# Optimization experiments

Measured on AMD Instinct MI355X. Metric: run time of the kernel, lower is better.

The kernel has to match this reference:

```python
import jax, jax.numpy as jnp
import numpy as np

N_NODES = 50000
HIDDEN = 256
N_EDGES = 300000


def setup_inputs() -> dict:
    key = jax.random.key(0)
    k1, k2, k3, k4 = jax.random.split(key, 4)
    node_embeddings = jax.random.normal(k1, (N_NODES, HIDDEN), dtype=jnp.float32)
    edge_weights_index = jax.random.randint(k2, (2, N_EDGES), 0, N_NODES, dtype=jnp.int64)
    # lin1: Linear(2H -> H), lin2: Linear(H -> 1); jax convention [in, out]
    W1 = jax.random.normal(k3, (2 * HIDDEN, HIDDEN), dtype=jnp.float32) * (1.0 / np.sqrt(2 * HIDDEN))
    b1 = jnp.zeros((HIDDEN,), dtype=jnp.float32)
    W2 = jax.random.normal(k4, (HIDDEN, 1), dtype=jnp.float32) * (1.0 / np.sqrt(HIDDEN))
    b2 = jnp.zeros((1,), dtype=jnp.float32)
    return {"node_embeddings": node_embeddings, "edge_weights_index": edge_weights_index,
            "W1": W1, "b1": b1, "W2": W2, "b2": b2}


def reference(node_embeddings, edge_weights_index, W1, b1, W2, b2):
    src = edge_weights_index[0, :]
    trg = edge_weights_index[1, :]
    # Split W1 into src/trg halves: concat([s, t]) @ W1 == s @ W1s + t @ W1t.
    # Avoids materializing the [E, 2H] concatenated edge tensor.
    W1s, W1t = W1[:HIDDEN], W1[HIDDEN:]
    h = node_embeddings[src] @ W1s + node_embeddings[trg] @ W1t + b1  # [E, H]
    h = jax.nn.relu(h)
    prediction = h @ W2 + b2  # [E, 1]
    return prediction.reshape(-1)
```

## Files before the change

kernel.cpp:

```cpp
#include <hip/hip_runtime.h>
#include <hip/hip_bf16.h>

#define N_NODES 50000
#define HID     256
#define N_EDGES 300000
#define NT      32
#define NTILES  ((N_NODES + NT - 1) / NT)

typedef __attribute__((ext_vector_type(8))) short bf16x8;
typedef __attribute__((ext_vector_type(4))) float f32x4;

__device__ __forceinline__ unsigned short f2bf(float f) {
  unsigned int u = __float_as_uint(f);
  u = (u + 0x7FFFu + ((u >> 16) & 1u)) >> 16;
  return (unsigned short)u;
}
__device__ __forceinline__ float bflo(unsigned int u) { return __uint_as_float(u << 16); }
__device__ __forceinline__ float bfhi(unsigned int u) { return __uint_as_float(u & 0xFFFF0000u); }

__device__ __forceinline__ bf16x8 cvt8(float4 u, float4 v) {
  bf16x8 r;
  r[0] = (short)f2bf(u.x); r[1] = (short)f2bf(u.y);
  r[2] = (short)f2bf(u.z); r[3] = (short)f2bf(u.w);
  r[4] = (short)f2bf(v.x); r[5] = (short)f2bf(v.y);
  r[6] = (short)f2bf(v.z); r[7] = (short)f2bf(v.w);
  return r;
}

struct StageRegs { float4 a, b, c, d; };

__device__ __forceinline__ void load_tile(const float* __restrict__ E, int tile,
                                          int srow, int sg, StageRegs& s) {
  int grow = tile * NT + srow;
  if (grow < N_NODES) {
    const float4* p = reinterpret_cast<const float4*>(E + (size_t)grow * HID + sg * 8);
    s.a = p[0]; s.b = p[1]; s.c = p[32]; s.d = p[33];
  } else {
    s.a = s.b = s.c = s.d = make_float4(0.f, 0.f, 0.f, 0.f);
  }
}

__global__ __launch_bounds__(128) void pack_w_kernel(
    const float* __restrict__ W1, unsigned short* __restrict__ Wtf) {
  int k = blockIdx.x;
  int t = threadIdx.x;
  int half = t >> 6;
  int jj = (t & 63) * 4;
  const float4 v = *reinterpret_cast<const float4*>(
      W1 + (size_t)(half ? (HID + k) : k) * HID + jj);
  float vv[4] = {v.x, v.y, v.z, v.w};
#pragma unroll
  for (int e = 0; e < 4; ++e) {
    int j = half * HID + jj + e;
    int f    = (j >> 4) * 8 + (k >> 5);
    int lane = (j & 15) | (((k >> 3) & 3) << 4);
    int elem = k & 7;
    Wtf[f * 512 + lane * 8 + elem] = f2bf(vv[e]);
  }
}

__global__ __launch_bounds__(512, 2) void gemm_kernel(
    const float* __restrict__ E, const unsigned short* __restrict__ Wtf,
    const float* __restrict__ b1, unsigned short* __restrict__ P) {
  __shared__ alignas(16) char lds0[16384];
  __shared__ alignas(16) char lds1[16384];
  const int tid  = threadIdx.x;
  const int lane = tid & 63;
  const int w    = tid >> 6;

  bf16x8 a[4][8];
#pragma unroll
  for (int m = 0; m < 4; ++m)
#pragma unroll
    for (int kk = 0; kk < 8; ++kk)
      a[m][kk] = *reinterpret_cast<const bf16x8*>(
          Wtf + (((size_t)(w * 4 + m) * 8 + kk) << 9) + lane * 8);

  float4 bv[4];
#pragma unroll
  for (int m = 0; m < 4; ++m) {
    int fm = w * 4 + m;
    bv[m] = (fm < 16) ? *reinterpret_cast<const float4*>(b1 + fm * 16 + ((lane >> 4) << 2))
                      : make_float4(0.f, 0.f, 0.f, 0.f);
  }

  const int srow = tid >> 4;
  const int sg   = tid & 15;
  const int woff0 = srow * 512 + ((sg * 16) ^ ((srow & 7) << 4));
  const int woff1 = srow * 512 + (((sg + 16) * 16) ^ ((srow & 7) << 4));
  const int G = gridDim.x;

  auto write_tile = [&](char* buf, const StageRegs& s) {
    *reinterpret_cast<bf16x8*>(&buf[woff0]) = cvt8(s.a, s.b);
    *reinterpret_cast<bf16x8*>(&buf[woff1]) = cvt8(s.c, s.d);
  };

  auto compute_store = [&](const char* buf, int tt) {
    f32x4 acc[4][2] = {};
#pragma unroll
    for (int n = 0; n < 2; ++n) {
      int r   = n * 16 + (lane & 15);
      int rb  = r * 512;
      int sw  = (r & 7) << 4;
      int kb0 = (lane >> 4) << 4;
      bf16x8 bfr[8];
#pragma unroll
      for (int kk = 0; kk < 8; ++kk)
        bfr[kk] = *reinterpret_cast<const bf16x8*>(&buf[rb + ((kk * 64 + kb0) ^ sw)]);
#pragma unroll
      for (int kk = 0; kk < 8; ++kk)
#pragma unroll
        for (int m = 0; m < 4; ++m)
          acc[m][n] = __builtin_amdgcn_mfma_f32_16x16x32_bf16(a[m][kk], bfr[kk], acc[m][n], 0, 0, 0);
    }
#pragma unroll
    for (int m = 0; m < 4; ++m) {
      int pcb = (w * 4 + m) * 16 + ((lane >> 4) << 2);
#pragma unroll
      for (int n = 0; n < 2; ++n) {
        int node = tt * NT + n * 16 + (lane & 15);
        if (node < N_NODES) {
          ushort4 o;
          o.x = f2bf(acc[m][n][0] + bv[m].x);
          o.y = f2bf(acc[m][n][1] + bv[m].y);
          o.z = f2bf(acc[m][n][2] + bv[m].z);
          o.w = f2bf(acc[m][n][3] + bv[m].w);
          *reinterpret_cast<ushort4*>(P + (size_t)node * 512 + pcb) = o;
        }
      }
    }
  };

  int t = blockIdx.x;
  StageRegs sX, sY;
  load_tile(E, t, srow, sg, sX);
  if (t + G < NTILES) load_tile(E, t + G, srow, sg, sY);
  write_tile(lds0, sX);
  if (t + 2 * G < NTILES) load_tile(E, t + 2 * G, srow, sg, sX);
  __syncthreads();

  while (true) {
    compute_store(lds0, t);
    if (t + G >= NTILES) break;
    write_tile(lds1, sY);
    if (t + 3 * G < NTILES) load_tile(E, t + 3 * G, srow, sg, sY);
    __syncthreads();
    t += G;
    compute_store(lds1, t);
    if (t + G >= NTILES) break;
    write_tile(lds0, sX);
    if (t + 3 * G < NTILES) load_tile(E, t + 3 * G, srow, sg, sX);
    __syncthreads();
    t += G;
  }
}

__global__ __launch_bounds__(256) void edge_kernel(
    const int* __restrict__ idx, const unsigned short* __restrict__ P,
    const float* __restrict__ W2, const float* __restrict__ b2,
    float* __restrict__ out) {
  const int tid  = threadIdx.x;
  const int lane = tid & 63;
  const int l32  = lane & 31;
  const int half = lane >> 5;
  const int wv     = blockIdx.x * 4 + (tid >> 6);
  const int nwaves = gridDim.x * 4;
  const float4 w0 = *reinterpret_cast<const float4*>(W2 + l32 * 8);
  const float4 w1 = *reinterpret_cast<const float4*>(W2 + l32 * 8 + 4);
  const float bias = b2[0];

  auto dotrelu = [&](uint4 ua, uint4 ub) -> float {
    float h0 = fmaxf(bflo(ua.x) + bflo(ub.x), 0.f);
    float h1 = fmaxf(bfhi(ua.x) + bfhi(ub.x), 0.f);
    float h2 = fmaxf(bflo(ua.y) + bflo(ub.y), 0.f);
    float h3 = fmaxf(bfhi(ua.y) + bfhi(ub.y), 0.f);
    float h4 = fmaxf(bflo(ua.z) + bflo(ub.z), 0.f);
    float h5 = fmaxf(bfhi(ua.z) + bfhi(ub.z), 0.f);
    float h6 = fmaxf(bflo(ua.w) + bflo(ub.w), 0.f);
    float h7 = fmaxf(bfhi(ua.w) + bfhi(ub.w), 0.f);
    return h0 * w0.x + h1 * w0.y + h2 * w0.z + h3 * w0.w
         + h4 * w1.x + h5 * w1.y + h6 * w1.z + h7 * w1.w;
  };

  for (int ep = wv; ep < N_EDGES / 2; ep += 2 * nwaves) {
    int eA  = ep * 2 + half;
    int epB = ep + nwaves;
    bool hasB = (epB < N_EDGES / 2);
    int eB  = hasB ? (epB * 2 + half) : eA;
    int sA = idx[eA];
    int tA = idx[N_EDGES + eA];
    int sB = idx[eB];
    int tB = idx[N_EDGES + eB];
    uint4 uaA = *reinterpret_cast<const uint4*>(P + (size_t)sA * 512 + l32 * 8);
    uint4 ubA = *reinterpret_cast<const uint4*>(P + (size_t)tA * 512 + 256 + l32 * 8);
    uint4 uaB = *reinterpret_cast<const uint4*>(P + (size_t)sB * 512 + l32 * 8);
    uint4 ubB = *reinterpret_cast<const uint4*>(P + (size_t)tB * 512 + 256 + l32 * 8);
    float accA = dotrelu(uaA, ubA);
    float accB = dotrelu(uaB, ubB);
#pragma unroll
    for (int off = 1; off < 32; off <<= 1) {
      accA += __shfl_xor(accA, off, 64);
      accB += __shfl_xor(accB, off, 64);
    }
    if (l32 == 0) {
      out[eA] = accA + bias;
      if (hasB) out[eB] = accB + bias;
    }
  }
}

extern "C" void kernel_launch(void* const* d_in, const int* in_sizes, int n_in,
                              void* d_out, int out_size, void* d_ws, size_t ws_size,
                              hipStream_t stream) {
  const float* E   = (const float*)d_in[0];
  const int*   idx = (const int*)d_in[1];
  const float* W1  = (const float*)d_in[2];
  const float* b1  = (const float*)d_in[3];
  const float* W2  = (const float*)d_in[4];
  const float* b2  = (const float*)d_in[5];
  float* out = (float*)d_out;

  unsigned short* Wtf = (unsigned short*)d_ws;
  unsigned short* P   = (unsigned short*)((char*)d_ws + 512 * HID * 2);

  hipLaunchKernelGGL(pack_w_kernel, dim3(HID), dim3(128), 0, stream, W1, Wtf);
  hipLaunchKernelGGL(gemm_kernel, dim3(256), dim3(512), 0, stream, E, Wtf, b1, P);
  hipLaunchKernelGGL(edge_kernel, dim3(2048), dim3(256), 0, stream, idx, P, W2, b2, out);
}
```

Measured before the change: 82.94 us.

## Split projected node table into hidden-half regions and gather in two edge passes

The GEMM now writes its bf16 projections in two separate regions, one per half of the hidden dimension, each holding the source and target columns for that half. The edge computation becomes two launches. The first pass gathers the first half and stores a partial dot product per edge. The second pass gathers the second half, adds the stored partial and the bias, and writes the output. The aim is to halve the working set each gather pass touches so random row gathers hit cache more often. In exchange, the edge indices are read twice, a partial buffer is written and read back, there is an extra launch, and each gather is a smaller 256-byte segment.

```diff
diff --git a/kernel.cpp b/kernel.cpp
--- a/kernel.cpp
+++ b/kernel.cpp
@@ -115,7 +115,10 @@
     }
 #pragma unroll
     for (int m = 0; m < 4; ++m) {
-      int pcb = (w * 4 + m) * 16 + ((lane >> 4) << 2);
+      int j0 = (w * 4 + m) * 16 + ((lane >> 4) << 2);
+      int region   = (j0 >> 7) & 1;
+      int elem_off = ((j0 >> 8) << 7) + (j0 & 127);
+      size_t rbase = (size_t)region * ((size_t)N_NODES * 256);
 #pragma unroll
       for (int n = 0; n < 2; ++n) {
         int node = tt * NT + n * 16 + (lane & 15);
@@ -125,7 +128,7 @@
           o.y = f2bf(acc[m][n][1] + bv[m].y);
           o.z = f2bf(acc[m][n][2] + bv[m].z);
           o.w = f2bf(acc[m][n][3] + bv[m].w);
-          *reinterpret_cast<ushort4*>(P + (size_t)node * 512 + pcb) = o;
+          *reinterpret_cast<ushort4*>(P + rbase + (size_t)node * 256 + elem_off) = o;
         }
       }
     }
@@ -155,56 +158,35 @@
   }
 }
 
-__global__ __launch_bounds__(256) void edge_kernel(
-    const int* __restrict__ idx, const unsigned short* __restrict__ P,
-    const float* __restrict__ W2, const float* __restrict__ b2,
-    float* __restrict__ out) {
+__global__ __launch_bounds__(256) void edge_pass_kernel(
+    const int* __restrict__ idx, const unsigned short* __restrict__ Pp,
+    const float* __restrict__ W2seg, const float* __restrict__ b2,
+    float* __restrict__ part, float* __restrict__ out, int pass) {
   const int tid  = threadIdx.x;
   const int lane = tid & 63;
   const int l32  = lane & 31;
   const int half = lane >> 5;
   const int wv     = blockIdx.x * 4 + (tid >> 6);
   const int nwaves = gridDim.x * 4;
-  const float4 w0 = *reinterpret_cast<const float4*>(W2 + l32 * 8);
-  const float4 w1 = *reinterpret_cast<const float4*>(W2 + l32 * 8 + 4);
+  const float4 w2 = *reinterpret_cast<const float4*>(W2seg + l32 * 4);
   const float bias = b2[0];
-
-  auto dotrelu = [&](uint4 ua, uint4 ub) -> float {
+  for (int ep = wv; ep < N_EDGES / 2; ep += nwaves) {
+    int e = ep * 2 + half;
+    int s = idx[e];
+    int t = idx[N_EDGES + e];
+    uint2 ua = *reinterpret_cast<const uint2*>(Pp + (size_t)s * 256 + l32 * 4);
+    uint2 ub = *reinterpret_cast<const uint2*>(Pp + (size_t)t * 256 + 128 + l32 * 4);
     float h0 = fmaxf(bflo(ua.x) + bflo(ub.x), 0.f);
     float h1 = fmaxf(bfhi(ua.x) + bfhi(ub.x), 0.f);
     float h2 = fmaxf(bflo(ua.y) + bflo(ub.y), 0.f);
     float h3 = fmaxf(bfhi(ua.y) + bfhi(ub.y), 0.f);
-    float h4 = fmaxf(bflo(ua.z) + bflo(ub.z), 0.f);
-    float h5 = fmaxf(bfhi(ua.z) + bfhi(ub.z), 0.f);
-    float h6 = fmaxf(bflo(ua.w) + bflo(ub.w), 0.f);
-    float h7 = fmaxf(bfhi(ua.w) + bfhi(ub.w), 0.f);
-    return h0 * w0.x + h1 * w0.y + h2 * w0.z + h3 * w0.w
-         + h4 * w1.x + h5 * w1.y + h6 * w1.z + h7 * w1.w;
-  };
-
-  for (int ep = wv; ep < N_EDGES / 2; ep += 2 * nwaves) {
-    int eA  = ep * 2 + half;
-    int epB = ep + nwaves;
-    bool hasB = (epB < N_EDGES / 2);
-    int eB  = hasB ? (epB * 2 + half) : eA;
-    int sA = idx[eA];
-    int tA = idx[N_EDGES + eA];
-    int sB = idx[eB];
-    int tB = idx[N_EDGES + eB];
-    uint4 uaA = *reinterpret_cast<const uint4*>(P + (size_t)sA * 512 + l32 * 8);
-    uint4 ubA = *reinterpret_cast<const uint4*>(P + (size_t)tA * 512 + 256 + l32 * 8);
-    uint4 uaB = *reinterpret_cast<const uint4*>(P + (size_t)sB * 512 + l32 * 8);
-    uint4 ubB = *reinterpret_cast<const uint4*>(P + (size_t)tB * 512 + 256 + l32 * 8);
-    float accA = dotrelu(uaA, ubA);
-    float accB = dotrelu(uaB, ubB);
-#pragma unroll
-    for (int off = 1; off < 32; off <<= 1) {
-      accA += __shfl_xor(accA, off, 64);
-      accB += __shfl_xor(accB, off, 64);
-    }
+    float acc = h0 * w2.x + h1 * w2.y + h2 * w2.z + h3 * w2.w;
+#pragma unroll
+    for (int off = 1; off < 32; off <<= 1)
+      acc += __shfl_xor(acc, off, 64);
     if (l32 == 0) {
-      out[eA] = accA + bias;
-      if (hasB) out[eB] = accB + bias;
+      if (pass == 0) part[e] = acc;
+      else           out[e]  = acc + part[e] + bias;
     }
   }
 }
@@ -220,10 +202,15 @@
   const float* b2  = (const float*)d_in[5];
   float* out = (float*)d_out;
 
-  unsigned short* Wtf = (unsigned short*)d_ws;
-  unsigned short* P   = (unsigned short*)((char*)d_ws + 512 * HID * 2);
+  char* ws = (char*)d_ws;
+  unsigned short* Wtf = (unsigned short*)ws;
+  unsigned short* P   = (unsigned short*)(ws + 262144);
+  float* part = (float*)(ws + 262144 + 51200000);
 
   hipLaunchKernelGGL(pack_w_kernel, dim3(HID), dim3(128), 0, stream, W1, Wtf);
   hipLaunchKernelGGL(gemm_kernel, dim3(256), dim3(512), 0, stream, E, Wtf, b1, P);
-  hipLaunchKernelGGL(edge_kernel, dim3(2048), dim3(256), 0, stream, idx, P, W2, b2, out);
-}
+  hipLaunchKernelGGL(edge_pass_kernel, dim3(2048), dim3(256), 0, stream,
+                     idx, P, W2, b2, part, out, 0);
+  hipLaunchKernelGGL(edge_pass_kernel, dim3(2048), dim3(256), 0, stream,
+                     idx, P + (size_t)N_NODES * 256, W2 + 128, b2, part, out, 1);
+}
```

Measured after the change: 96.84 us. 16.8% more time.

## Split GEMM work over 1024-thread blocks and simplify edge loop

Applied to the files above, without the earlier changes.

The node GEMM now runs with 16 waves per block. Each wave holds 2 W1 column fragments instead of 4, which halves per-wave weight registers and accumulators, and each thread stages one 8-float chunk per tile instead of two. The launch bound asks for 4 such blocks per CU, which forces a tight register cap and may cause spills. The edge kernel drops its two-edges-per-iteration unrolling and processes one edge pair per wave iteration, which is simpler but exposes less memory-level parallelism in the gather.

```diff
diff --git a/kernel.cpp b/kernel.cpp
--- a/kernel.cpp
+++ b/kernel.cpp
@@ -27,18 +27,7 @@
   return r;
 }
 
-struct StageRegs { float4 a, b, c, d; };
-
-__device__ __forceinline__ void load_tile(const float* __restrict__ E, int tile,
-                                          int srow, int sg, StageRegs& s) {
-  int grow = tile * NT + srow;
-  if (grow < N_NODES) {
-    const float4* p = reinterpret_cast<const float4*>(E + (size_t)grow * HID + sg * 8);
-    s.a = p[0]; s.b = p[1]; s.c = p[32]; s.d = p[33];
-  } else {
-    s.a = s.b = s.c = s.d = make_float4(0.f, 0.f, 0.f, 0.f);
-  }
-}
+struct StageRegs { float4 a, b; };
 
 __global__ __launch_bounds__(128) void pack_w_kernel(
     const float* __restrict__ W1, unsigned short* __restrict__ Wtf) {
@@ -59,7 +48,7 @@
   }
 }
 
-__global__ __launch_bounds__(512, 2) void gemm_kernel(
+__global__ __launch_bounds__(1024, 4) void gemm_kernel(
     const float* __restrict__ E, const unsigned short* __restrict__ Wtf,
     const float* __restrict__ b1, unsigned short* __restrict__ P) {
   __shared__ alignas(16) char lds0[16384];
@@ -68,35 +57,42 @@
   const int lane = tid & 63;
   const int w    = tid >> 6;
 
-  bf16x8 a[4][8];
-#pragma unroll
-  for (int m = 0; m < 4; ++m)
+  bf16x8 a[2][8];
+#pragma unroll
+  for (int m = 0; m < 2; ++m)
 #pragma unroll
     for (int kk = 0; kk < 8; ++kk)
       a[m][kk] = *reinterpret_cast<const bf16x8*>(
-          Wtf + (((size_t)(w * 4 + m) * 8 + kk) << 9) + lane * 8);
-
-  float4 bv[4];
-#pragma unroll
-  for (int m = 0; m < 4; ++m) {
-    int fm = w * 4 + m;
+          Wtf + (((size_t)(w * 2 + m) * 8 + kk) << 9) + lane * 8);
+
+  float4 bv[2];
+#pragma unroll
+  for (int m = 0; m < 2; ++m) {
+    int fm = w * 2 + m;
     bv[m] = (fm < 16) ? *reinterpret_cast<const float4*>(b1 + fm * 16 + ((lane >> 4) << 2))
                       : make_float4(0.f, 0.f, 0.f, 0.f);
   }
 
-  const int srow = tid >> 4;
-  const int sg   = tid & 15;
-  const int woff0 = srow * 512 + ((sg * 16) ^ ((srow & 7) << 4));
-  const int woff1 = srow * 512 + (((sg + 16) * 16) ^ ((srow & 7) << 4));
+  const int srow = tid >> 5;
+  const int sg   = tid & 31;
+  const int woff = srow * 512 + ((sg * 16) ^ ((srow & 7) << 4));
   const int G = gridDim.x;
 
+  auto load_tile = [&](int tile, StageRegs& s) {
+    int grow = tile * NT + srow;
+    if (grow < N_NODES) {
+      const float4* p = reinterpret_cast<const float4*>(E + (size_t)grow * HID + sg * 8);
+      s.a = p[0]; s.b = p[1];
+    } else {
+      s.a = s.b = make_float4(0.f, 0.f, 0.f, 0.f);
+    }
+  };
   auto write_tile = [&](char* buf, const StageRegs& s) {
-    *reinterpret_cast<bf16x8*>(&buf[woff0]) = cvt8(s.a, s.b);
-    *reinterpret_cast<bf16x8*>(&buf[woff1]) = cvt8(s.c, s.d);
+    *reinterpret_cast<bf16x8*>(&buf[woff]) = cvt8(s.a, s.b);
   };
 
   auto compute_store = [&](const char* buf, int tt) {
-    f32x4 acc[4][2] = {};
+    f32x4 acc[2][2] = {};
 #pragma unroll
     for (int n = 0; n < 2; ++n) {
       int r   = n * 16 + (lane & 15);
@@ -110,12 +106,12 @@
 #pragma unroll
       for (int kk = 0; kk < 8; ++kk)
 #pragma unroll
-        for (int m = 0; m < 4; ++m)
+        for (int m = 0; m < 2; ++m)
           acc[m][n] = __builtin_amdgcn_mfma_f32_16x16x32_bf16(a[m][kk], bfr[kk], acc[m][n], 0, 0, 0);
     }
 #pragma unroll
-    for (int m = 0; m < 4; ++m) {
-      int pcb = (w * 4 + m) * 16 + ((lane >> 4) << 2);
+    for (int m = 0; m < 2; ++m) {
+      int pcb = (w * 2 + m) * 16 + ((lane >> 4) << 2);
 #pragma unroll
       for (int n = 0; n < 2; ++n) {
         int node = tt * NT + n * 16 + (lane & 15);
@@ -133,23 +129,23 @@
 
   int t = blockIdx.x;
   StageRegs sX, sY;
-  load_tile(E, t, srow, sg, sX);
-  if (t + G < NTILES) load_tile(E, t + G, srow, sg, sY);
+  load_tile(t, sX);
+  if (t + G < NTILES) load_tile(t + G, sY);
   write_tile(lds0, sX);
-  if (t + 2 * G < NTILES) load_tile(E, t + 2 * G, srow, sg, sX);
+  if (t + 2 * G < NTILES) load_tile(t + 2 * G, sX);
   __syncthreads();
 
   while (true) {
     compute_store(lds0, t);
     if (t + G >= NTILES) break;
     write_tile(lds1, sY);
-    if (t + 3 * G < NTILES) load_tile(E, t + 3 * G, srow, sg, sY);
+    if (t + 3 * G < NTILES) load_tile(t + 3 * G, sY);
     __syncthreads();
     t += G;
     compute_store(lds1, t);
     if (t + G >= NTILES) break;
     write_tile(lds0, sX);
-    if (t + 3 * G < NTILES) load_tile(E, t + 3 * G, srow, sg, sX);
+    if (t + 3 * G < NTILES) load_tile(t + 3 * G, sX);
     __syncthreads();
     t += G;
   }
@@ -168,8 +164,12 @@
   const float4 w0 = *reinterpret_cast<const float4*>(W2 + l32 * 8);
   const float4 w1 = *reinterpret_cast<const float4*>(W2 + l32 * 8 + 4);
   const float bias = b2[0];
-
-  auto dotrelu = [&](uint4 ua, uint4 ub) -> float {
+  for (int ep = wv; ep < N_EDGES / 2; ep += nwaves) {
+    int e = ep * 2 + half;
+    int s = idx[e];
+    int t = idx[N_EDGES + e];
+    uint4 ua = *reinterpret_cast<const uint4*>(P + (size_t)s * 512 + l32 * 8);
+    uint4 ub = *reinterpret_cast<const uint4*>(P + (size_t)t * 512 + 256 + l32 * 8);
     float h0 = fmaxf(bflo(ua.x) + bflo(ub.x), 0.f);
     float h1 = fmaxf(bfhi(ua.x) + bfhi(ub.x), 0.f);
     float h2 = fmaxf(bflo(ua.y) + bflo(ub.y), 0.f);
@@ -178,34 +178,12 @@
     float h5 = fmaxf(bfhi(ua.z) + bfhi(ub.z), 0.f);
     float h6 = fmaxf(bflo(ua.w) + bflo(ub.w), 0.f);
     float h7 = fmaxf(bfhi(ua.w) + bfhi(ub.w), 0.f);
-    return h0 * w0.x + h1 * w0.y + h2 * w0.z + h3 * w0.w
-         + h4 * w1.x + h5 * w1.y + h6 * w1.z + h7 * w1.w;
-  };
-
-  for (int ep = wv; ep < N_EDGES / 2; ep += 2 * nwaves) {
-    int eA  = ep * 2 + half;
-    int epB = ep + nwaves;
-    bool hasB = (epB < N_EDGES / 2);
-    int eB  = hasB ? (epB * 2 + half) : eA;
-    int sA = idx[eA];
-    int tA = idx[N_EDGES + eA];
-    int sB = idx[eB];
-    int tB = idx[N_EDGES + eB];
-    uint4 uaA = *reinterpret_cast<const uint4*>(P + (size_t)sA * 512 + l32 * 8);
-    uint4 ubA = *reinterpret_cast<const uint4*>(P + (size_t)tA * 512 + 256 + l32 * 8);
-    uint4 uaB = *reinterpret_cast<const uint4*>(P + (size_t)sB * 512 + l32 * 8);
-    uint4 ubB = *reinterpret_cast<const uint4*>(P + (size_t)tB * 512 + 256 + l32 * 8);
-    float accA = dotrelu(uaA, ubA);
-    float accB = dotrelu(uaB, ubB);
-#pragma unroll
-    for (int off = 1; off < 32; off <<= 1) {
-      accA += __shfl_xor(accA, off, 64);
-      accB += __shfl_xor(accB, off, 64);
-    }
-    if (l32 == 0) {
-      out[eA] = accA + bias;
-      if (hasB) out[eB] = accB + bias;
-    }
+    float acc = h0 * w0.x + h1 * w0.y + h2 * w0.z + h3 * w0.w
+              + h4 * w1.x + h5 * w1.y + h6 * w1.z + h7 * w1.w;
+#pragma unroll
+    for (int off = 1; off < 32; off <<= 1)
+      acc += __shfl_xor(acc, off, 64);
+    if (l32 == 0) out[e] = acc + bias;
   }
 }
 
@@ -221,9 +199,9 @@
   float* out = (float*)d_out;
 
   unsigned short* Wtf = (unsigned short*)d_ws;
-  unsigned short* P   = (unsigned short*)((char*)d_ws + 512 * HID * 2);
+  unsigned short* P   = (unsigned short*)((char*)d_ws + 262144);
 
   hipLaunchKernelGGL(pack_w_kernel, dim3(HID), dim3(128), 0, stream, W1, Wtf);
-  hipLaunchKernelGGL(gemm_kernel, dim3(256), dim3(512), 0, stream, E, Wtf, b1, P);
+  hipLaunchKernelGGL(gemm_kernel, dim3(256), dim3(1024), 0, stream, E, Wtf, b1, P);
   hipLaunchKernelGGL(edge_kernel, dim3(2048), dim3(256), 0, stream, idx, P, W2, b2, out);
 }
```

Measured after the change: 83.14 us. Within noise of the previous version (+0.2%).
